# Kernel tuning notes

Measured on AMD Instinct MI355X. Metric: run time of the kernel, lower is better.

The kernel has to match this reference:

```python
import jax, jax.numpy as jnp
import numpy as np

NP, P, H, NB = 14, 16, 12, 6  # n_patches per side, patch size, heads, blocks
HD, EMB, SEQ = 64, 768, NP * NP + 1


def _layernorm(x, g, b, eps=1e-5):
    m = x.mean(axis=-1, keepdims=True)
    v = x.var(axis=-1, keepdims=True)
    return (x - m) * jax.lax.rsqrt(v + eps) * g + b


def setup_inputs() -> dict:
    key = jax.random.key(0)
    ks = jax.random.split(key, 16)
    s = 0.02
    B = 64
    inp = {
        "images": jax.random.normal(ks[0], (B, 3, 224, 224), jnp.float32),
        "Wmap": jax.random.normal(ks[1], (768, 768), jnp.float32) * s,
        "bmap": jnp.zeros((768,), jnp.float32),
        "cls_tok": jax.random.normal(ks[2], (1, 768), jnp.float32) * s,
        "pos": jax.random.normal(ks[3], (SEQ, 768), jnp.float32) * s,
        "ln1_g": jnp.ones((NB, 768), jnp.float32),
        "ln1_b": jnp.zeros((NB, 768), jnp.float32),
        "Wq": jax.random.normal(ks[4], (NB, H, HD, HD), jnp.float32) * s,
        "bq": jnp.zeros((NB, H, HD), jnp.float32),
        "Wk": jax.random.normal(ks[5], (NB, H, HD, HD), jnp.float32) * s,
        "bk": jnp.zeros((NB, H, HD), jnp.float32),
        "Wv": jax.random.normal(ks[6], (NB, H, HD, HD), jnp.float32) * s,
        "bv": jnp.zeros((NB, H, HD), jnp.float32),
        "ln2_g": jnp.ones((NB, 768), jnp.float32),
        "ln2_b": jnp.zeros((NB, 768), jnp.float32),
        "W1": jax.random.normal(ks[7], (NB, 768, 3072), jnp.float32) * s,
        "b1": jnp.zeros((NB, 3072), jnp.float32),
        "W2": jax.random.normal(ks[8], (NB, 3072, 768), jnp.float32) * s,
        "b2": jnp.zeros((NB, 768), jnp.float32),
        "Whead": jax.random.normal(ks[9], (768, 10), jnp.float32) * s,
        "bhead": jnp.zeros((10,), jnp.float32),
    }
    return inp


def reference(images, Wmap, bmap, cls_tok, pos, ln1_g, ln1_b, Wq, bq, Wk, bk,
              Wv, bv, ln2_g, ln2_b, W1, b1, W2, b2, Whead, bhead):
    B = images.shape[0]
    # patchify: (B,3,224,224) -> (B,196,768); per-patch channel-first flatten
    x = images.reshape(B, 3, NP, P, NP, P)
    x = x.transpose(0, 2, 4, 1, 3, 5).reshape(B, NP * NP, 3 * P * P)
    tokens = x @ Wmap + bmap  # (B,196,768)
    tokens = jnp.concatenate(
        [jnp.broadcast_to(cls_tok[None], (B, 1, EMB)), tokens], axis=1)
    out = tokens + pos[None]  # (B,197,768)
    scale = 1.0 / jnp.sqrt(jnp.asarray(H, out.dtype))  # NOTE: source divides by sqrt(num_heads)
    for i in range(NB):
        h = _layernorm(out, ln1_g[i], ln1_b[i])
        xh = h.reshape(B, SEQ, H, HD)
        q = jnp.einsum('bshd,hde->bshe', xh, Wq[i]) + bq[i]
        k = jnp.einsum('bshd,hde->bshe', xh, Wk[i]) + bk[i]
        v = jnp.einsum('bshd,hde->bshe', xh, Wv[i]) + bv[i]
        attn = jax.nn.softmax(
            jnp.einsum('bqhd,bkhd->bhqk', q, k) * scale, axis=-1)
        o = jnp.einsum('bhqk,bkhd->bqhd', attn, v).reshape(B, SEQ, EMB)
        out = out + o
        h2 = _layernorm(out, ln2_g[i], ln2_b[i])
        mlp = jax.nn.gelu(h2 @ W1[i] + b1[i], approximate=False) @ W2[i] + b2[i]
        out = out + mlp
    cls = out[:, 0]  # (B,768)
    return jax.nn.softmax(cls @ Whead + bhead, axis=-1)
```

## Files before the change

### kernel.cpp

```cpp
#include <hip/hip_runtime.h>
#include <cstddef>

#define BATCH 64
#define SEQL  197
#define EMB   768
#define NH    12
#define HDIM  64
#define NBLK  6
#define MLPD  3072
#define TOKS  12608
#define PTOK  12544
#define ATT_SCALE 0.28867513459481287f
#define LOG2E 1.4426950408889634f

typedef short bf16x8 __attribute__((ext_vector_type(8)));
typedef float f32x4  __attribute__((ext_vector_type(4)));

__device__ inline float bf2f(unsigned short u) {
  union { unsigned int i; float f; } c; c.i = ((unsigned int)u) << 16; return c.f;
}
__device__ inline unsigned short f2bf(float f) {
  union { float f; unsigned int i; } c; c.f = f;
  unsigned int r = c.i + 0x7FFFu + ((c.i >> 16) & 1u);
  return (unsigned short)(r >> 16);
}

__device__ __forceinline__ void gload16(const unsigned short* g, void* l) {
  __builtin_amdgcn_global_load_lds(
      (const __attribute__((address_space(1))) unsigned int*)g,
      (__attribute__((address_space(3))) unsigned int*)l, 16, 0, 0);
}

__global__ __launch_bounds__(256) void patchify_kernel(const float* __restrict__ img,
                                                       unsigned short* __restrict__ out) {
  int i4 = blockIdx.x * 256 + threadIdx.x;
  int f4 = i4 % 192;
  int r  = i4 / 192;
  int b  = r / 196, t = r - b * 196;
  int f  = f4 * 4;
  int c  = f >> 8;
  int rem = f & 255;
  int iy = rem >> 4, ix = rem & 15;
  int py = t / 14, px = t - py * 14;
  const float* src = img + ((((size_t)b * 3 + c) * 224 + py * 16 + iy) * 224 + px * 16 + ix);
  float4 v = *(const float4*)src;
  ushort4 u;
  u.x = f2bf(v.x); u.y = f2bf(v.y); u.z = f2bf(v.z); u.w = f2bf(v.w);
  *(ushort4*)(out + (size_t)r * 768 + f) = u;
}

__global__ __launch_bounds__(256) void clspos_kernel(const float* __restrict__ cls,
                                                     const float* __restrict__ pos,
                                                     float* __restrict__ X) {
  int idx = blockIdx.x * 256 + threadIdx.x;
  int b = idx / 768, e = idx - b * 768;
  X[(size_t)b * SEQL * 768 + e] = cls[e] + pos[e];
}

__global__ __launch_bounds__(256) void wconv_kernel(const float* __restrict__ W,
                                                    unsigned short* __restrict__ Wt,
                                                    int K, int N) {
  __shared__ float t[32][33];
  int k0 = blockIdx.x * 32, n0 = blockIdx.y * 32;
  int kk = threadIdx.x >> 3, nn = (threadIdx.x & 7) * 4;
  float4 v = *(const float4*)&W[(size_t)(k0 + kk) * N + n0 + nn];
  t[nn + 0][kk] = v.x; t[nn + 1][kk] = v.y; t[nn + 2][kk] = v.z; t[nn + 3][kk] = v.w;
  __syncthreads();
  int nr = threadIdx.x >> 3, kc = (threadIdx.x & 7) * 4;
  ushort4 u;
  u.x = f2bf(t[nr][kc + 0]); u.y = f2bf(t[nr][kc + 1]);
  u.z = f2bf(t[nr][kc + 2]); u.w = f2bf(t[nr][kc + 3]);
  *(ushort4*)&Wt[(size_t)(n0 + nr) * K + k0 + kc] = u;
}

template<int MODE>
__global__ __launch_bounds__(256) void gemm_mfma(const unsigned short* __restrict__ A, int lda,
                                                 const unsigned short* __restrict__ Bt, int ldb,
                                                 void* __restrict__ Cv,
                                                 const float* __restrict__ bias,
                                                 const float* __restrict__ pos,
                                                 int M, int N, int K) {
  __shared__ short As[8192];
  __shared__ short Bs[8192];
  const int tid  = threadIdx.x;
  const int wid  = tid >> 6, lane = tid & 63;
  const int wr   = wid >> 1, wc = wid & 1;
  const int fr   = lane & 15;
  const int fq   = lane >> 4;
  const int m0   = blockIdx.y * 128;
  const int n0   = blockIdx.x * 128;
  const int srow = lane >> 3;
  const int schk = lane & 7;
  const int Mc   = M - 1;

  f32x4 acc[4][4];
#pragma unroll
  for (int m = 0; m < 4; ++m)
#pragma unroll
    for (int n = 0; n < 4; ++n) acc[m][n] = (f32x4)0.f;

  for (int k0 = 0; k0 < K; k0 += 64) {
#pragma unroll
    for (int i = 0; i < 4; ++i) {
      int row = i * 32 + wid * 8 + srow;
      int gr = m0 + row; if (gr > Mc) gr = Mc;
      gload16(A + (size_t)gr * lda + k0 + ((schk ^ (row & 7)) << 3),
              (char*)As + i * 4096 + wid * 1024);
      gload16(Bt + (size_t)(n0 + row) * ldb + k0 + ((schk ^ (row & 7)) << 3),
              (char*)Bs + i * 4096 + wid * 1024);
    }
    __syncthreads();
#pragma unroll
    for (int ks = 0; ks < 2; ++ks) {
      bf16x8 af[4], bfr[4];
#pragma unroll
      for (int m = 0; m < 4; ++m) {
        int row = (wr << 6) + (m << 4) + fr;
        int ch = ((ks << 2) + fq) ^ (row & 7);
        af[m] = *(const bf16x8*)&As[(row << 6) + (ch << 3)];
      }
#pragma unroll
      for (int n = 0; n < 4; ++n) {
        int row = (wc << 6) + (n << 4) + fr;
        int ch = ((ks << 2) + fq) ^ (row & 7);
        bfr[n] = *(const bf16x8*)&Bs[(row << 6) + (ch << 3)];
      }
#pragma unroll
      for (int m = 0; m < 4; ++m)
#pragma unroll
        for (int n = 0; n < 4; ++n)
          acc[m][n] = __builtin_amdgcn_mfma_f32_16x16x32_bf16(af[m], bfr[n], acc[m][n], 0, 0, 0);
    }
    __syncthreads();
  }

#pragma unroll
  for (int m = 0; m < 4; ++m) {
#pragma unroll
    for (int j = 0; j < 4; ++j) {
      int r = m0 + (wr << 6) + (m << 4) + (fq << 2) + j;
      if (r >= M) continue;
#pragma unroll
      for (int n = 0; n < 4; ++n) {
        int c = n0 + (wc << 6) + (n << 4) + fr;
        float v = acc[m][n][j] + bias[c];
        if (MODE == 0) {
          int b = r / 196, t = r - b * 196;
          ((float*)Cv)[((size_t)b * SEQL + 1 + t) * 768 + c] = v + pos[(size_t)(1 + t) * 768 + c];
        } else if (MODE == 1) {
          float g = 0.5f * v * (1.f + erff(v * 0.70710678118654752f));
          ((unsigned short*)Cv)[(size_t)r * MLPD + c] = f2bf(g);
        } else {
          ((float*)Cv)[(size_t)r * 768 + c] += v;
        }
      }
    }
  }
}

__global__ __launch_bounds__(256) void ln_kernel(const float* __restrict__ Xi,
                                                 unsigned short* __restrict__ Ho,
                                                 const float* __restrict__ g,
                                                 const float* __restrict__ bb) {
  int tok = blockIdx.x * 4 + (threadIdx.x >> 6);
  int lane = threadIdx.x & 63;
  const float* x = Xi + (size_t)tok * 768;
  float4 v0 = *(const float4*)(x + lane * 4);
  float4 v1 = *(const float4*)(x + 256 + lane * 4);
  float4 v2 = *(const float4*)(x + 512 + lane * 4);
  float s = v0.x + v0.y + v0.z + v0.w + v1.x + v1.y + v1.z + v1.w + v2.x + v2.y + v2.z + v2.w;
  float q = v0.x*v0.x + v0.y*v0.y + v0.z*v0.z + v0.w*v0.w
          + v1.x*v1.x + v1.y*v1.y + v1.z*v1.z + v1.w*v1.w
          + v2.x*v2.x + v2.y*v2.y + v2.z*v2.z + v2.w*v2.w;
#pragma unroll
  for (int o = 32; o > 0; o >>= 1) { s += __shfl_xor(s, o); q += __shfl_xor(q, o); }
  float mean = s * (1.f / 768.f);
  float var  = q * (1.f / 768.f) - mean * mean;
  float rs = rsqrtf(var + 1e-5f);
  unsigned short* outp = Ho + (size_t)tok * 768;
  float4 g0 = *(const float4*)(g + lane * 4);
  float4 g1 = *(const float4*)(g + 256 + lane * 4);
  float4 g2 = *(const float4*)(g + 512 + lane * 4);
  float4 b0 = *(const float4*)(bb + lane * 4);
  float4 b1 = *(const float4*)(bb + 256 + lane * 4);
  float4 b2 = *(const float4*)(bb + 512 + lane * 4);
  ushort4 s0, s1, s2;
  s0.x = f2bf((v0.x - mean) * rs * g0.x + b0.x); s0.y = f2bf((v0.y - mean) * rs * g0.y + b0.y);
  s0.z = f2bf((v0.z - mean) * rs * g0.z + b0.z); s0.w = f2bf((v0.w - mean) * rs * g0.w + b0.w);
  s1.x = f2bf((v1.x - mean) * rs * g1.x + b1.x); s1.y = f2bf((v1.y - mean) * rs * g1.y + b1.y);
  s1.z = f2bf((v1.z - mean) * rs * g1.z + b1.z); s1.w = f2bf((v1.w - mean) * rs * g1.w + b1.w);
  s2.x = f2bf((v2.x - mean) * rs * g2.x + b2.x); s2.y = f2bf((v2.y - mean) * rs * g2.y + b2.y);
  s2.z = f2bf((v2.z - mean) * rs * g2.z + b2.z); s2.w = f2bf((v2.w - mean) * rs * g2.w + b2.w);
  *(ushort4*)(outp + lane * 4) = s0;
  *(ushort4*)(outp + 256 + lane * 4) = s1;
  *(ushort4*)(outp + 512 + lane * 4) = s2;
}

__global__ __launch_bounds__(256) void qkv_kernel(const unsigned short* __restrict__ Hb,
    const float* __restrict__ Wq, const float* __restrict__ bq,
    const float* __restrict__ Wk, const float* __restrict__ bk,
    const float* __restrict__ Wv, const float* __restrict__ bv,
    unsigned short* __restrict__ Qo, unsigned short* __restrict__ Ko,
    unsigned short* __restrict__ Vo) {
  __shared__ float xs[32][68];
  __shared__ float ws[3][64][64];
  const int h = blockIdx.y;
  const int tk0 = blockIdx.x * 32;
  const int tid = threadIdx.x;
  {
    int tok = tid >> 3;
    int p = (tid & 7) * 8;
    const unsigned short* src = Hb + (size_t)(tk0 + tok) * 768 + h * 64 + p;
    ushort4 u0 = *(const ushort4*)src;
    ushort4 u1 = *(const ushort4*)(src + 4);
    xs[tok][p + 0] = bf2f(u0.x); xs[tok][p + 1] = bf2f(u0.y);
    xs[tok][p + 2] = bf2f(u0.z); xs[tok][p + 3] = bf2f(u0.w);
    xs[tok][p + 4] = bf2f(u1.x); xs[tok][p + 5] = bf2f(u1.y);
    xs[tok][p + 6] = bf2f(u1.z); xs[tok][p + 7] = bf2f(u1.w);
  }
  {
    const float* w0 = Wq + (size_t)h * 4096;
    const float* w1 = Wk + (size_t)h * 4096;
    const float* w2 = Wv + (size_t)h * 4096;
    int base = tid * 16;
    float* wf = &ws[0][0][0];
#pragma unroll
    for (int j = 0; j < 16; j += 4) {
      *(float4*)(wf + base + j)        = *(const float4*)(w0 + base + j);
      *(float4*)(wf + 4096 + base + j) = *(const float4*)(w1 + base + j);
      *(float4*)(wf + 8192 + base + j) = *(const float4*)(w2 + base + j);
    }
  }
  __syncthreads();
  const int e4 = (tid & 15) * 4;
  const int t2 = (tid >> 4) * 2;
  float acc[3][2][4];
#pragma unroll
  for (int m = 0; m < 3; ++m)
#pragma unroll
    for (int ti = 0; ti < 2; ++ti)
#pragma unroll
      for (int j = 0; j < 4; ++j) acc[m][ti][j] = 0.f;

#pragma unroll 4
  for (int d4 = 0; d4 < 16; ++d4) {
    float x0[4], x1[4];
    *(float4*)x0 = *(float4*)&xs[t2][d4 * 4];
    *(float4*)x1 = *(float4*)&xs[t2 + 1][d4 * 4];
#pragma unroll
    for (int m = 0; m < 3; ++m)
#pragma unroll
      for (int dj = 0; dj < 4; ++dj) {
        float4 w = *(float4*)&ws[m][d4 * 4 + dj][e4];
        acc[m][0][0] += x0[dj] * w.x; acc[m][0][1] += x0[dj] * w.y;
        acc[m][0][2] += x0[dj] * w.z; acc[m][0][3] += x0[dj] * w.w;
        acc[m][1][0] += x1[dj] * w.x; acc[m][1][1] += x1[dj] * w.y;
        acc[m][1][2] += x1[dj] * w.z; acc[m][1][3] += x1[dj] * w.w;
      }
  }
#pragma unroll
  for (int m = 0; m < 3; ++m) {
    const float* bptr = (m == 0 ? bq : (m == 1 ? bk : bv)) + h * 64 + e4;
    unsigned short* optr = (m == 0 ? Qo : (m == 1 ? Ko : Vo));
    const float sc = (m == 0) ? ATT_SCALE : 1.f;
#pragma unroll
    for (int ti = 0; ti < 2; ++ti) {
      int tk = tk0 + t2 + ti;
      int b = tk / 197, s = tk - b * 197;
      size_t base_o = (((size_t)b * NH + h) * SEQL + s) * 64 + e4;
      ushort4 o;
      o.x = f2bf((acc[m][ti][0] + bptr[0]) * sc);
      o.y = f2bf((acc[m][ti][1] + bptr[1]) * sc);
      o.z = f2bf((acc[m][ti][2] + bptr[2]) * sc);
      o.w = f2bf((acc[m][ti][3] + bptr[3]) * sc);
      *(ushort4*)&optr[base_o] = o;
    }
  }
}

__global__ __launch_bounds__(256) void attn_kernel(const unsigned short* __restrict__ Q,
                                                   const unsigned short* __restrict__ Kg,
                                                   const unsigned short* __restrict__ Vg,
                                                   float* __restrict__ X) {
  __shared__ unsigned short Vt[64][232];
  __shared__ unsigned short Pl[4][16][232];
  const int bh = blockIdx.x;
  const int b = bh / NH, h = bh - b * NH;
  const int tid = threadIdx.x, wv = tid >> 6, lane = tid & 63;
  const int fr = lane & 15, hi = lane >> 4;
  const unsigned short* Qp = Q  + (size_t)bh * SEQL * 64;
  const unsigned short* Kp = Kg + (size_t)bh * SEQL * 64;
  const unsigned short* Vp = Vg + (size_t)bh * SEQL * 64;

  for (int idx = tid; idx < SEQL * 16; idx += 256) {
    int s = idx >> 4, d4 = (idx & 15) * 4;
    ushort4 v = *(const ushort4*)&Vp[s * 64 + d4];
    Vt[d4 + 0][s] = v.x; Vt[d4 + 1][s] = v.y; Vt[d4 + 2][s] = v.z; Vt[d4 + 3][s] = v.w;
  }
  for (int idx = tid; idx < 64 * 35; idx += 256) {
    int d = idx / 35, c = 197 + idx % 35;
    Vt[d][c] = 0;
  }
  for (int idx = lane; idx < 16 * 24; idx += 64) {
    int r = idx / 24, c = 208 + idx % 24;
    Pl[wv][r][c] = 0;
  }
  __syncthreads();

  for (int qt = wv; qt < 13; qt += 4) {
    int qrow = qt * 16 + fr; if (qrow > 196) qrow = 196;
    bf16x8 qa0 = *(const bf16x8*)&Qp[qrow * 64 + hi * 8];
    bf16x8 qa1 = *(const bf16x8*)&Qp[qrow * 64 + 32 + hi * 8];
    f32x4 sc[13];
#pragma unroll
    for (int kt = 0; kt < 13; ++kt) {
      int krow = kt * 16 + fr; if (krow > 196) krow = 196;
      bf16x8 kb0 = *(const bf16x8*)&Kp[krow * 64 + hi * 8];
      bf16x8 kb1 = *(const bf16x8*)&Kp[krow * 64 + 32 + hi * 8];
      f32x4 a = (f32x4)0.f;
      a = __builtin_amdgcn_mfma_f32_16x16x32_bf16(qa0, kb0, a, 0, 0, 0);
      a = __builtin_amdgcn_mfma_f32_16x16x32_bf16(qa1, kb1, a, 0, 0, 0);
      sc[kt] = a;
    }
    float mx[4] = {-3e38f, -3e38f, -3e38f, -3e38f};
#pragma unroll
    for (int kt = 0; kt < 13; ++kt) {
      bool inval = (kt == 12) && (fr >= 5);
#pragma unroll
      for (int j = 0; j < 4; ++j) {
        float s = inval ? -3e38f : sc[kt][j];
        sc[kt][j] = s;
        mx[j] = fmaxf(mx[j], s);
      }
    }
#pragma unroll
    for (int o = 8; o > 0; o >>= 1)
#pragma unroll
      for (int j = 0; j < 4; ++j) mx[j] = fmaxf(mx[j], __shfl_xor(mx[j], o));
    float l[4] = {0.f, 0.f, 0.f, 0.f};
#pragma unroll
    for (int kt = 0; kt < 13; ++kt) {
#pragma unroll
      for (int j = 0; j < 4; ++j) {
        float p = exp2f((sc[kt][j] - mx[j]) * LOG2E);
        if ((kt == 12) && (fr >= 5)) p = 0.f;
        l[j] += p;
        Pl[wv][hi * 4 + j][kt * 16 + fr] = f2bf(p);
      }
    }
#pragma unroll
    for (int o = 8; o > 0; o >>= 1)
#pragma unroll
      for (int j = 0; j < 4; ++j) l[j] += __shfl_xor(l[j], o);
    f32x4 ov[4];
#pragma unroll
    for (int n = 0; n < 4; ++n) ov[n] = (f32x4)0.f;
#pragma unroll
    for (int kc = 0; kc < 7; ++kc) {
      bf16x8 pa = *(const bf16x8*)&Pl[wv][fr][kc * 32 + hi * 8];
#pragma unroll
      for (int n = 0; n < 4; ++n) {
        bf16x8 vb = *(const bf16x8*)&Vt[n * 16 + fr][kc * 32 + hi * 8];
        ov[n] = __builtin_amdgcn_mfma_f32_16x16x32_bf16(pa, vb, ov[n], 0, 0, 0);
      }
    }
#pragma unroll
    for (int j = 0; j < 4; ++j) {
      int r = qt * 16 + hi * 4 + j;
      if (r >= SEQL) continue;
      float inv = 1.f / l[j];
      float* xp = X + ((size_t)b * SEQL + r) * 768 + h * 64 + fr;
#pragma unroll
      for (int n = 0; n < 4; ++n) xp[n * 16] += ov[n][j] * inv;
    }
  }
}

__global__ __launch_bounds__(64) void head_kernel(const float* __restrict__ X,
                                                  const float* __restrict__ Wh,
                                                  const float* __restrict__ bh,
                                                  float* __restrict__ out) {
  __shared__ float lg[10];
  int b = blockIdx.x, t = threadIdx.x;
  if (t < 10) {
    float acc = bh[t];
    const float* x = X + (size_t)b * SEQL * 768;
    for (int d = 0; d < 768; ++d) acc += x[d] * Wh[d * 10 + t];
    lg[t] = acc;
  }
  __syncthreads();
  if (t == 0) {
    float m = lg[0];
    for (int c = 1; c < 10; ++c) m = fmaxf(m, lg[c]);
    float ssum = 0.f;
    for (int c = 0; c < 10; ++c) ssum += expf(lg[c] - m);
    for (int c = 0; c < 10; ++c) out[b * 10 + c] = expf(lg[c] - m) / ssum;
  }
}

extern "C" void kernel_launch(void* const* d_in, const int* in_sizes, int n_in,
                              void* d_out, int out_size, void* d_ws, size_t ws_size,
                              hipStream_t stream) {
  const float* images = (const float*)d_in[0];
  const float* Wmap = (const float*)d_in[1];
  const float* bmap = (const float*)d_in[2];
  const float* cls  = (const float*)d_in[3];
  const float* pos  = (const float*)d_in[4];
  const float* ln1g = (const float*)d_in[5];
  const float* ln1b = (const float*)d_in[6];
  const float* Wq   = (const float*)d_in[7];
  const float* bq   = (const float*)d_in[8];
  const float* Wk   = (const float*)d_in[9];
  const float* bk   = (const float*)d_in[10];
  const float* Wv   = (const float*)d_in[11];
  const float* bv   = (const float*)d_in[12];
  const float* ln2g = (const float*)d_in[13];
  const float* ln2b = (const float*)d_in[14];
  const float* W1   = (const float*)d_in[15];
  const float* b1   = (const float*)d_in[16];
  const float* W2   = (const float*)d_in[17];
  const float* b2   = (const float*)d_in[18];
  const float* Wh   = (const float*)d_in[19];
  const float* bhd  = (const float*)d_in[20];
  float* out = (float*)d_out;

  const size_t ACT = (size_t)TOKS * 768;
  const size_t oX = 0;
  const size_t oHb = oX + ACT * 4;
  const size_t oR  = oHb + ACT * 2;
  const size_t oW1 = oR + 3 * ACT * 4;
  const size_t oW2 = oW1 + (size_t)768 * 3072 * 2;
  const size_t oWm = oW2 + (size_t)768 * 3072 * 2;
  const size_t need = oWm + (size_t)768 * 768 * 2;
  if (ws_size < need) return;

  char* ws = (char*)d_ws;
  float* X = (float*)(ws + oX);
  unsigned short* Hb = (unsigned short*)(ws + oHb);
  unsigned short* Qb = (unsigned short*)(ws + oR);
  unsigned short* Kb = Qb + ACT;
  unsigned short* Vb = Kb + ACT;
  unsigned short* mid = (unsigned short*)(ws + oR);
  unsigned short* patches = (unsigned short*)(ws + oR);
  unsigned short* W1t = (unsigned short*)(ws + oW1);
  unsigned short* W2t = (unsigned short*)(ws + oW2);
  unsigned short* Wmapt = (unsigned short*)(ws + oWm);

  wconv_kernel<<<dim3(24, 24), 256, 0, stream>>>(Wmap, Wmapt, 768, 768);
  patchify_kernel<<<9408, 256, 0, stream>>>(images, patches);
  clspos_kernel<<<192, 256, 0, stream>>>(cls, pos, X);
  gemm_mfma<0><<<dim3(6, 98), 256, 0, stream>>>(patches, 768, Wmapt, 768, X, bmap, pos,
                                                PTOK, 768, 768);

  for (int i = 0; i < NBLK; ++i) {
    ln_kernel<<<3152, 256, 0, stream>>>(X, Hb, ln1g + i * 768, ln1b + i * 768);
    qkv_kernel<<<dim3(394, 12), 256, 0, stream>>>(Hb,
        Wq + (size_t)i * 49152, bq + i * 768,
        Wk + (size_t)i * 49152, bk + i * 768,
        Wv + (size_t)i * 49152, bv + i * 768, Qb, Kb, Vb);
    attn_kernel<<<768, 256, 0, stream>>>(Qb, Kb, Vb, X);
    ln_kernel<<<3152, 256, 0, stream>>>(X, Hb, ln2g + i * 768, ln2b + i * 768);
    wconv_kernel<<<dim3(24, 96), 256, 0, stream>>>(W1 + (size_t)i * 2359296, W1t, 768, MLPD);
    wconv_kernel<<<dim3(96, 24), 256, 0, stream>>>(W2 + (size_t)i * 2359296, W2t, MLPD, 768);
    gemm_mfma<1><<<dim3(24, 99), 256, 0, stream>>>(Hb, 768, W1t, 768, mid, b1 + i * MLPD,
                                                   nullptr, TOKS, MLPD, 768);
    gemm_mfma<2><<<dim3(6, 99), 256, 0, stream>>>(mid, MLPD, W2t, MLPD, X, b2 + i * 768,
                                                  nullptr, TOKS, 768, MLPD);
  }
  head_kernel<<<64, 64, 0, stream>>>(X, Wh, bhd, out);
}
```

Baseline: 2.150 ms.

## Double-buffer GEMM LDS tiles and move per-head QKV projection to MFMA

The main bf16 GEMM now uses two LDS buffers and issues the next K-tile's loads before computing on the current one, waiting with a partial vmcnt so memory traffic overlaps the MFMA work. It also sets launch_bounds(256,2). Separately, the per-head QKV projection is replaced with an MFMA kernel that reads pre-transposed bf16 weights, produced by a new small conversion kernel each block. Together these target exposed global-load latency in the GEMMs and the scalar FP32 FMA cost of the QKV step, at the price of doubled LDS use per block and an extra tiny launch.

Measured after the change: 2.360 ms. 9.8% more time.

```diff
diff --git a/kernel.cpp b/kernel.cpp
--- a/kernel.cpp
+++ b/kernel.cpp
@@ -73,15 +73,29 @@
   *(ushort4*)&Wt[(size_t)(n0 + nr) * K + k0 + kc] = u;
 }
 
+__global__ __launch_bounds__(256) void qwconv_kernel(const float* __restrict__ Wq,
+                                                     const float* __restrict__ Wk,
+                                                     const float* __restrict__ Wv,
+                                                     unsigned short* __restrict__ Wt) {
+  int mh = blockIdx.x;
+  int m = mh / 12, h = mh - m * 12;
+  const float* src = (m == 0 ? Wq : (m == 1 ? Wk : Wv)) + (size_t)h * 4096;
+  unsigned short* dst = Wt + (size_t)mh * 4096;
+  for (int idx = threadIdx.x; idx < 4096; idx += 256) {
+    int d = idx >> 6, e = idx & 63;
+    dst[e * 64 + d] = f2bf(src[idx]);
+  }
+}
+
 template<int MODE>
-__global__ __launch_bounds__(256) void gemm_mfma(const unsigned short* __restrict__ A, int lda,
-                                                 const unsigned short* __restrict__ Bt, int ldb,
-                                                 void* __restrict__ Cv,
-                                                 const float* __restrict__ bias,
-                                                 const float* __restrict__ pos,
-                                                 int M, int N, int K) {
-  __shared__ short As[8192];
-  __shared__ short Bs[8192];
+__global__ __launch_bounds__(256, 2) void gemm_mfma(const unsigned short* __restrict__ A, int lda,
+                                                    const unsigned short* __restrict__ Bt, int ldb,
+                                                    void* __restrict__ Cv,
+                                                    const float* __restrict__ bias,
+                                                    const float* __restrict__ pos,
+                                                    int M, int N, int K) {
+  __shared__ short As[2][8192];
+  __shared__ short Bs[2][8192];
   const int tid  = threadIdx.x;
   const int wid  = tid >> 6, lane = tid & 63;
   const int wr   = wid >> 1, wc = wid & 1;
@@ -92,6 +106,7 @@
   const int srow = lane >> 3;
   const int schk = lane & 7;
   const int Mc   = M - 1;
+  const int T    = K >> 6;
 
   f32x4 acc[4][4];
 #pragma unroll
@@ -99,17 +114,29 @@
 #pragma unroll
     for (int n = 0; n < 4; ++n) acc[m][n] = (f32x4)0.f;
 
-  for (int k0 = 0; k0 < K; k0 += 64) {
+  auto STAGE = [&](int bufi, int k0) {
 #pragma unroll
     for (int i = 0; i < 4; ++i) {
       int row = i * 32 + wid * 8 + srow;
       int gr = m0 + row; if (gr > Mc) gr = Mc;
       gload16(A + (size_t)gr * lda + k0 + ((schk ^ (row & 7)) << 3),
-              (char*)As + i * 4096 + wid * 1024);
+              (char*)&As[bufi][0] + i * 4096 + wid * 1024);
       gload16(Bt + (size_t)(n0 + row) * ldb + k0 + ((schk ^ (row & 7)) << 3),
-              (char*)Bs + i * 4096 + wid * 1024);
-    }
-    __syncthreads();
+              (char*)&Bs[bufi][0] + i * 4096 + wid * 1024);
+    }
+  };
+
+  STAGE(0, 0);
+  for (int t = 0; t < T; ++t) {
+    const int c = t & 1;
+    if (t + 1 < T) {
+      STAGE(c ^ 1, (t + 1) << 6);
+      asm volatile("s_waitcnt vmcnt(8)" ::: "memory");
+    } else {
+      asm volatile("s_waitcnt vmcnt(0)" ::: "memory");
+    }
+    __builtin_amdgcn_s_barrier();
+    __builtin_amdgcn_sched_barrier(0);
 #pragma unroll
     for (int ks = 0; ks < 2; ++ks) {
       bf16x8 af[4], bfr[4];
@@ -117,13 +144,13 @@
       for (int m = 0; m < 4; ++m) {
         int row = (wr << 6) + (m << 4) + fr;
         int ch = ((ks << 2) + fq) ^ (row & 7);
-        af[m] = *(const bf16x8*)&As[(row << 6) + (ch << 3)];
+        af[m] = *(const bf16x8*)&As[c][(row << 6) + (ch << 3)];
       }
 #pragma unroll
       for (int n = 0; n < 4; ++n) {
         int row = (wc << 6) + (n << 4) + fr;
         int ch = ((ks << 2) + fq) ^ (row & 7);
-        bfr[n] = *(const bf16x8*)&Bs[(row << 6) + (ch << 3)];
+        bfr[n] = *(const bf16x8*)&Bs[c][(row << 6) + (ch << 3)];
       }
 #pragma unroll
       for (int m = 0; m < 4; ++m)
@@ -131,7 +158,8 @@
         for (int n = 0; n < 4; ++n)
           acc[m][n] = __builtin_amdgcn_mfma_f32_16x16x32_bf16(af[m], bfr[n], acc[m][n], 0, 0, 0);
     }
-    __syncthreads();
+    __builtin_amdgcn_sched_barrier(0);
+    __builtin_amdgcn_s_barrier();
   }
 
 #pragma unroll
@@ -196,84 +224,47 @@
   *(ushort4*)(outp + 512 + lane * 4) = s2;
 }
 
-__global__ __launch_bounds__(256) void qkv_kernel(const unsigned short* __restrict__ Hb,
-    const float* __restrict__ Wq, const float* __restrict__ bq,
-    const float* __restrict__ Wk, const float* __restrict__ bk,
-    const float* __restrict__ Wv, const float* __restrict__ bv,
+__global__ __launch_bounds__(256) void qkv_mfma(const unsigned short* __restrict__ Hb,
+    const unsigned short* __restrict__ Wt,
+    const float* __restrict__ bq, const float* __restrict__ bk, const float* __restrict__ bv,
     unsigned short* __restrict__ Qo, unsigned short* __restrict__ Ko,
     unsigned short* __restrict__ Vo) {
-  __shared__ float xs[32][68];
-  __shared__ float ws[3][64][64];
   const int h = blockIdx.y;
-  const int tk0 = blockIdx.x * 32;
-  const int tid = threadIdx.x;
-  {
-    int tok = tid >> 3;
-    int p = (tid & 7) * 8;
-    const unsigned short* src = Hb + (size_t)(tk0 + tok) * 768 + h * 64 + p;
-    ushort4 u0 = *(const ushort4*)src;
-    ushort4 u1 = *(const ushort4*)(src + 4);
-    xs[tok][p + 0] = bf2f(u0.x); xs[tok][p + 1] = bf2f(u0.y);
-    xs[tok][p + 2] = bf2f(u0.z); xs[tok][p + 3] = bf2f(u0.w);
-    xs[tok][p + 4] = bf2f(u1.x); xs[tok][p + 5] = bf2f(u1.y);
-    xs[tok][p + 6] = bf2f(u1.z); xs[tok][p + 7] = bf2f(u1.w);
-  }
-  {
-    const float* w0 = Wq + (size_t)h * 4096;
-    const float* w1 = Wk + (size_t)h * 4096;
-    const float* w2 = Wv + (size_t)h * 4096;
-    int base = tid * 16;
-    float* wf = &ws[0][0][0];
-#pragma unroll
-    for (int j = 0; j < 16; j += 4) {
-      *(float4*)(wf + base + j)        = *(const float4*)(w0 + base + j);
-      *(float4*)(wf + 4096 + base + j) = *(const float4*)(w1 + base + j);
-      *(float4*)(wf + 8192 + base + j) = *(const float4*)(w2 + base + j);
-    }
-  }
-  __syncthreads();
-  const int e4 = (tid & 15) * 4;
-  const int t2 = (tid >> 4) * 2;
-  float acc[3][2][4];
+  const int tid = threadIdx.x, wv = tid >> 6, lane = tid & 63;
+  const int fr = lane & 15, hi = lane >> 4;
+  const int t0 = blockIdx.x * 64 + wv * 16;
+  const unsigned short* arow = Hb + (size_t)(t0 + fr) * 768 + h * 64;
+  bf16x8 a0 = *(const bf16x8*)(arow + hi * 8);
+  bf16x8 a1 = *(const bf16x8*)(arow + 32 + hi * 8);
+  f32x4 acc[3][4];
 #pragma unroll
   for (int m = 0; m < 3; ++m)
 #pragma unroll
-    for (int ti = 0; ti < 2; ++ti)
-#pragma unroll
-      for (int j = 0; j < 4; ++j) acc[m][ti][j] = 0.f;
-
-#pragma unroll 4
-  for (int d4 = 0; d4 < 16; ++d4) {
-    float x0[4], x1[4];
-    *(float4*)x0 = *(float4*)&xs[t2][d4 * 4];
-    *(float4*)x1 = *(float4*)&xs[t2 + 1][d4 * 4];
-#pragma unroll
-    for (int m = 0; m < 3; ++m)
-#pragma unroll
-      for (int dj = 0; dj < 4; ++dj) {
-        float4 w = *(float4*)&ws[m][d4 * 4 + dj][e4];
-        acc[m][0][0] += x0[dj] * w.x; acc[m][0][1] += x0[dj] * w.y;
-        acc[m][0][2] += x0[dj] * w.z; acc[m][0][3] += x0[dj] * w.w;
-        acc[m][1][0] += x1[dj] * w.x; acc[m][1][1] += x1[dj] * w.y;
-        acc[m][1][2] += x1[dj] * w.z; acc[m][1][3] += x1[dj] * w.w;
-      }
-  }
+    for (int n = 0; n < 4; ++n) acc[m][n] = (f32x4)0.f;
 #pragma unroll
   for (int m = 0; m < 3; ++m) {
-    const float* bptr = (m == 0 ? bq : (m == 1 ? bk : bv)) + h * 64 + e4;
+    const unsigned short* wb = Wt + (size_t)(m * 12 + h) * 4096;
+#pragma unroll
+    for (int n = 0; n < 4; ++n) {
+      bf16x8 b0 = *(const bf16x8*)&wb[(n * 16 + fr) * 64 + hi * 8];
+      bf16x8 b1 = *(const bf16x8*)&wb[(n * 16 + fr) * 64 + 32 + hi * 8];
+      acc[m][n] = __builtin_amdgcn_mfma_f32_16x16x32_bf16(a0, b0, acc[m][n], 0, 0, 0);
+      acc[m][n] = __builtin_amdgcn_mfma_f32_16x16x32_bf16(a1, b1, acc[m][n], 0, 0, 0);
+    }
+  }
+#pragma unroll
+  for (int m = 0; m < 3; ++m) {
+    const float* bptr = (m == 0 ? bq : (m == 1 ? bk : bv)) + h * 64;
     unsigned short* optr = (m == 0 ? Qo : (m == 1 ? Ko : Vo));
     const float sc = (m == 0) ? ATT_SCALE : 1.f;
 #pragma unroll
-    for (int ti = 0; ti < 2; ++ti) {
-      int tk = tk0 + t2 + ti;
+    for (int j = 0; j < 4; ++j) {
+      int tk = t0 + hi * 4 + j;
       int b = tk / 197, s = tk - b * 197;
-      size_t base_o = (((size_t)b * NH + h) * SEQL + s) * 64 + e4;
-      ushort4 o;
-      o.x = f2bf((acc[m][ti][0] + bptr[0]) * sc);
-      o.y = f2bf((acc[m][ti][1] + bptr[1]) * sc);
-      o.z = f2bf((acc[m][ti][2] + bptr[2]) * sc);
-      o.w = f2bf((acc[m][ti][3] + bptr[3]) * sc);
-      *(ushort4*)&optr[base_o] = o;
+      size_t base_o = (((size_t)b * NH + h) * SEQL + s) * 64;
+#pragma unroll
+      for (int n = 0; n < 4; ++n)
+        optr[base_o + n * 16 + fr] = f2bf((acc[m][n][j] + bptr[n * 16 + fr]) * sc);
     }
   }
 }
@@ -431,7 +422,8 @@
   const size_t oW1 = oR + 3 * ACT * 4;
   const size_t oW2 = oW1 + (size_t)768 * 3072 * 2;
   const size_t oWm = oW2 + (size_t)768 * 3072 * 2;
-  const size_t need = oWm + (size_t)768 * 768 * 2;
+  const size_t oQW = oWm + (size_t)768 * 768 * 2;
+  const size_t need = oQW + (size_t)36 * 4096 * 2;
   if (ws_size < need) return;
 
   char* ws = (char*)d_ws;
@@ -445,6 +437,7 @@
   unsigned short* W1t = (unsigned short*)(ws + oW1);
   unsigned short* W2t = (unsigned short*)(ws + oW2);
   unsigned short* Wmapt = (unsigned short*)(ws + oWm);
+  unsigned short* QWt = (unsigned short*)(ws + oQW);
 
   wconv_kernel<<<dim3(24, 24), 256, 0, stream>>>(Wmap, Wmapt, 768, 768);
   patchify_kernel<<<9408, 256, 0, stream>>>(images, patches);
@@ -454,10 +447,10 @@
 
   for (int i = 0; i < NBLK; ++i) {
     ln_kernel<<<3152, 256, 0, stream>>>(X, Hb, ln1g + i * 768, ln1b + i * 768);
-    qkv_kernel<<<dim3(394, 12), 256, 0, stream>>>(Hb,
-        Wq + (size_t)i * 49152, bq + i * 768,
-        Wk + (size_t)i * 49152, bk + i * 768,
-        Wv + (size_t)i * 49152, bv + i * 768, Qb, Kb, Vb);
+    qwconv_kernel<<<36, 256, 0, stream>>>(Wq + (size_t)i * 49152, Wk + (size_t)i * 49152,
+                                          Wv + (size_t)i * 49152, QWt);
+    qkv_mfma<<<dim3(197, 12), 256, 0, stream>>>(Hb, QWt,
+        bq + i * 768, bk + i * 768, bv + i * 768, Qb, Kb, Vb);
     attn_kernel<<<768, 256, 0, stream>>>(Qb, Kb, Vb, X);
     ln_kernel<<<3152, 256, 0, stream>>>(X, Hb, ln2g + i * 768, ln2b + i * 768);
     wconv_kernel<<<dim3(24, 96), 256, 0, stream>>>(W1 + (size_t)i * 2359296, W1t, 768, MLPD);
```
